# Performance work log

Hardware: AMD Instinct MI355X
Metric: run time of the kernel (lower is better)

The kernel has to match this reference:

```python
import jax, jax.numpy as jnp
import numpy as np

EPS = 1e-8
PHI = (1 + 5 ** 0.5) / 2
B, S, D, H, L, O = 8, 2048, 256, 512, 3, 1
NH = 4
HD = H // NH


def setup_inputs() -> dict:
    key = jax.random.key(0)
    ks = jax.random.split(key, 12)
    g = lambda k, shape, s=0.02: jax.random.normal(k, shape, dtype=jnp.float32) * s
    # Fibonacci modular spiral embedding (fixed, requires_grad=False in torch)
    idx = jnp.arange(D, dtype=jnp.float32)
    r = (PHI * idx) % 1.0
    th = 2 * jnp.pi * r
    phase_emb = jnp.stack([r * jnp.cos(th), r * jnp.sin(th)], axis=1)  # [D,2]
    return dict(
        x=jax.random.normal(ks[0], (B, S, D), dtype=jnp.float32),
        proj_w=g(ks[1], (D, D), 0.06), proj_b=jnp.zeros((D,), jnp.float32),
        phase_emb=phase_emb,
        hebb_w=g(ks[2], (H, 2), 0.5),
        attn_in_w=g(ks[3], (L, 3 * H, H)), attn_in_b=jnp.zeros((L, 3 * H), jnp.float32),
        attn_out_w=g(ks[4], (L, H, H)), attn_out_b=jnp.zeros((L, H), jnp.float32),
        ff1_w=g(ks[5], (L, 4 * H, H)), ff1_b=jnp.zeros((L, 4 * H), jnp.float32),
        ff2_w=g(ks[6], (L, H, 4 * H)), ff2_b=jnp.zeros((L, H), jnp.float32),
        ln1_w=jnp.ones((L, H), jnp.float32), ln1_b=jnp.zeros((L, H), jnp.float32),
        ln2_w=jnp.ones((L, H), jnp.float32), ln2_b=jnp.zeros((L, H), jnp.float32),
        normA_w=jnp.ones((H,), jnp.float32), normA_b=jnp.zeros((H,), jnp.float32),
        normB_w=jnp.ones((H // 2,), jnp.float32), normB_b=jnp.zeros((H // 2,), jnp.float32),
        p1_w=g(ks[7], (H // 2, H), 0.04), p1_b=jnp.zeros((H // 2,), jnp.float32),
        p2_w=g(ks[8], (O, H // 2), 0.06), p2_b=jnp.zeros((O,), jnp.float32),
    )


def _ln(x, w, b, eps=1e-5):
    m = x.mean(-1, keepdims=True)
    v = ((x - m) ** 2).mean(-1, keepdims=True)
    return (x - m) * jax.lax.rsqrt(v + eps) * w + b


def _diffuse(psi, mask, dt, steps):
    # Norm-preserving RK2 integration of d(psi)/dt = mask@psi - psi
    def force(state):
        return jnp.einsum('bij,bjd->bid', mask, state) - state

    def step(p, _):
        r = jnp.linalg.norm(p, axis=-1, keepdims=True)
        k1 = force(p)
        ps = p + dt * k1
        ps = ps * (r / (jnp.linalg.norm(ps, axis=-1, keepdims=True) + EPS))
        k2 = force(ps)
        pn = p + 0.5 * dt * (k1 + k2)
        pn = pn * (r / (jnp.linalg.norm(pn, axis=-1, keepdims=True) + EPS))
        return pn, None

    psi, _ = jax.lax.scan(step, psi, None, length=steps)
    return psi


def _forward(x, proj_w, proj_b, phase_emb, hebb_w, attn_in_w, attn_in_b,
             attn_out_w, attn_out_b, ff1_w, ff1_b, ff2_w, ff2_b,
             ln1_w, ln1_b, ln2_w, ln2_b, normA_w, normA_b, normB_w, normB_b,
             p1_w, p1_b, p2_w, p2_b):
    b, s, _ = x.shape
    # PhaseHebbianEmbedder: project then map to 2D phase coords, unit-normalize
    xp = x @ proj_w.T + proj_b                               # [B,S,D]
    pc = jnp.einsum('bsd,dt->bst', xp, phase_emb)            # [B,S,2]
    psi = pc / (jnp.linalg.norm(pc, axis=-1, keepdims=True) + EPS)
    mask = jnp.broadcast_to(jnp.eye(s, dtype=x.dtype), (b, s, s))  # [B,S,S]
    psi = _diffuse(psi, mask, 0.1, 3)
    psi = _diffuse(psi, mask, 0.05, 4)
    A = jnp.einsum('bsd,btd->bst', psi, psi)                 # [B,S,S]
    final_psi = psi[:, -1]                                   # [B,2]
    h = (final_psi @ hebb_w.T)[:, None, :]                   # [B,1,H]
    for l in range(attn_in_w.shape[0]):
        qkv = h @ attn_in_w[l].T + attn_in_b[l]
        q, k, v = jnp.split(qkv, 3, axis=-1)
        hd = lambda t: t.reshape(b, -1, NH, HD).transpose(0, 2, 1, 3)
        q, k, v = hd(q), hd(k), hd(v)
        sc = jnp.einsum('bhqd,bhkd->bhqk', q, k) / jnp.sqrt(jnp.float32(HD))
        att = jax.nn.softmax(sc, axis=-1)
        o = jnp.einsum('bhqk,bhkd->bhqd', att, v).transpose(0, 2, 1, 3).reshape(b, -1, H)
        o = o @ attn_out_w[l].T + attn_out_b[l]
        h = _ln(h + o, ln1_w[l], ln1_b[l])
        ff = jax.nn.silu(h @ ff1_w[l].T + ff1_b[l]) @ ff2_w[l].T + ff2_b[l]
        h = _ln(h + ff, ln2_w[l], ln2_b[l])
    h = _ln(h[:, 0, :], normA_w, normA_b)
    p = jax.nn.silu(h @ p1_w.T + p1_b)
    p = _ln(p, normB_w, normB_b)
    preds = p @ p2_w.T + p2_b                                # [B,O]
    return preds, A, mask, psi


def reference(x, proj_w, proj_b, phase_emb, hebb_w, attn_in_w, attn_in_b,
              attn_out_w, attn_out_b, ff1_w, ff1_b, ff2_w, ff2_b,
              ln1_w, ln1_b, ln2_w, ln2_b, normA_w, normA_b, normB_w, normB_b,
              p1_w, p1_b, p2_w, p2_b):
    return _forward(x, proj_w, proj_b, phase_emb, hebb_w, attn_in_w, attn_in_b,
                    attn_out_w, attn_out_b, ff1_w, ff1_b, ff2_w, ff2_b,
                    ln1_w, ln1_b, ln2_w, ln2_b, normA_w, normA_b,
                    normB_w, normB_b, p1_w, p1_b, p2_w, p2_b)
```

## Files before the change

kernel.cpp:

```cpp
#include <hip/hip_runtime.h>
#include <hip/hip_bf16.h>

#define BB 8
#define SS 2048
#define DD 256
#define HH 512
#define LL 3
#define NROWS (BB * SS)

typedef float floatx4 __attribute__((ext_vector_type(4)));

__device__ __forceinline__ void amask_row(const float* __restrict__ psi,
                                          float* __restrict__ A, float* __restrict__ M,
                                          int blk)
{
    int tid = threadIdx.x;
    int b = blk >> 11, i = blk & (SS - 1);
    float2 pi = *reinterpret_cast<const float2*>(psi + (size_t)blk * 2);
    #pragma unroll
    for (int c = 0; c < 2; ++c) {
        int j0 = c * 1024 + tid * 4;
        const float4* pr = reinterpret_cast<const float4*>(psi + ((size_t)b * SS + j0) * 2);
        float4 q0 = pr[0], q1 = pr[1];
        floatx4 o;
        o.x = pi.x * q0.x + pi.y * q0.y;
        o.y = pi.x * q0.z + pi.y * q0.w;
        o.z = pi.x * q1.x + pi.y * q1.y;
        o.w = pi.x * q1.z + pi.y * q1.w;
        size_t rb = (size_t)blk * SS + j0;
        __builtin_nontemporal_store(o, reinterpret_cast<floatx4*>(A + rb));
        floatx4 m;
        m.x = (i == j0    ) ? 1.f : 0.f;
        m.y = (i == j0 + 1) ? 1.f : 0.f;
        m.z = (i == j0 + 2) ? 1.f : 0.f;
        m.w = (i == j0 + 3) ? 1.f : 0.f;
        __builtin_nontemporal_store(m, reinterpret_cast<floatx4*>(M + rb));
    }
}

__global__ void compute_M(const float* __restrict__ pw, const float* __restrict__ pb,
                          const float* __restrict__ pe, float* __restrict__ Mc)
{
    __shared__ float s0[4][256], s1[4][256];
    int tid = threadIdx.x;
    int k = tid & 255;
    int sub = tid >> 8;
    float a0 = 0.f, a1 = 0.f;
    #pragma unroll 8
    for (int d = sub * 64; d < sub * 64 + 64; ++d) {
        float w = pw[d * DD + k];
        a0 += w * pe[2 * d];
        a1 += w * pe[2 * d + 1];
    }
    s0[sub][k] = a0;
    s1[sub][k] = a1;
    __syncthreads();
    if (tid < 256) {
        Mc[2 * tid]     = s0[0][tid] + s0[1][tid] + s0[2][tid] + s0[3][tid];
        Mc[2 * tid + 1] = s1[0][tid] + s1[1][tid] + s1[2][tid] + s1[3][tid];
    }
    if (tid < 64) {
        float c0 = 0.f, c1 = 0.f;
        for (int d = tid; d < DD; d += 64) {
            c0 += pb[d] * pe[2 * d];
            c1 += pb[d] * pe[2 * d + 1];
        }
        #pragma unroll
        for (int dd = 32; dd; dd >>= 1) {
            c0 += __shfl_xor(c0, dd);
            c1 += __shfl_xor(c1, dd);
        }
        if (tid == 0) { Mc[512] = c0; Mc[513] = c1; }
    }
}

__global__ void psi_kernel(const float* __restrict__ x, const float* __restrict__ Mc,
                           const float* __restrict__ hebb,
                           float* __restrict__ psi, float* __restrict__ T)
{
    __shared__ float sM[516];
    __shared__ float sH[2];
    int tid = threadIdx.x;
    for (int i = tid; i < 514; i += 256) sM[i] = Mc[i];
    __syncthreads();

    int sub = tid & 3;
    int rloc = tid >> 2;
    int rid = blockIdx.x * 64 + rloc;
    const float4* xr = reinterpret_cast<const float4*>(x + (size_t)rid * DD);
    float a0 = 0.f, a1 = 0.f;
    #pragma unroll
    for (int i = sub; i < DD / 4; i += 4) {
        float4 v = xr[i];
        int k2 = i * 8;
        a0 += v.x * sM[k2]     + v.y * sM[k2 + 2] + v.z * sM[k2 + 4] + v.w * sM[k2 + 6];
        a1 += v.x * sM[k2 + 1] + v.y * sM[k2 + 3] + v.z * sM[k2 + 5] + v.w * sM[k2 + 7];
    }
    a0 += __shfl_xor(a0, 1); a0 += __shfl_xor(a0, 2);
    a1 += __shfl_xor(a1, 1); a1 += __shfl_xor(a1, 2);

    bool leader = (sub == 0);
    float px = 0.f, py = 0.f;
    if (leader) {
        a0 += sM[512];
        a1 += sM[513];
        float n = sqrtf(a0 * a0 + a1 * a1);
        float scale = 1.f / (n + 1e-8f);
        float r = n * scale;
        #pragma unroll
        for (int it = 0; it < 7; ++it) {
            float f = r / (r + 1e-8f);
            scale *= f;
            r *= f;
        }
        px = a0 * scale;
        py = a1 * scale;
        float2 pv;
        pv.x = px;
        pv.y = py;
        *reinterpret_cast<float2*>(psi + (size_t)rid * 2) = pv;
    }

    if ((blockIdx.x & 31) == 31) {
        if (leader && rloc == 63) { sH[0] = px; sH[1] = py; }
        __syncthreads();
        float hx = sH[0], hy = sH[1];
        int b = blockIdx.x >> 5;
        T[(size_t)b * HH + tid]       = hx * hebb[2 * tid]         + hy * hebb[2 * tid + 1];
        T[(size_t)b * HH + tid + 256] = hx * hebb[2 * (tid + 256)] + hy * hebb[2 * (tid + 256) + 1];
    }
}

__global__ void head_mm(const float* __restrict__ X, int K,
                        const float* __restrict__ xlnw, const float* __restrict__ xlnb,
                        const float* __restrict__ W, const float* __restrict__ bias,
                        const float* __restrict__ res,
                        const float* __restrict__ reslnw, const float* __restrict__ reslnb,
                        float* __restrict__ out, int J, int G, int act,
                        const float* __restrict__ psi,
                        float* __restrict__ Ao, float* __restrict__ Mo,
                        int mmBlocks, int arow0)
{
    const int bid = blockIdx.x;
    if (bid >= mmBlocks) {
        int r = arow0 + (bid - mmBlocks);
        if (r < NROWS) amask_row(psi, Ao, Mo, r);
        return;
    }

    extern __shared__ float sX[];
    __shared__ float s_m[8], s_r[8], s_rm[8], s_rr[8];
    const int tid = threadIdx.x;
    const int row = tid >> 5, lane = tid & 31;
    const bool doLN = (xlnw != nullptr);
    const bool doRLN = (res != nullptr) && (reslnw != nullptr);

    if (doLN) {
        float s = 0.f, ss = 0.f;
        for (int k = lane; k < K; k += 32) {
            float v = X[row * K + k];
            s += v; ss += v * v;
        }
        for (int d = 16; d; d >>= 1) { s += __shfl_down(s, d); ss += __shfl_down(ss, d); }
        if (lane == 0) {
            float m = s / K;
            s_m[row] = m;
            s_r[row] = rsqrtf(ss / K - m * m + 1e-5f);
        }
    }
    if (doRLN) {
        float s = 0.f, ss = 0.f;
        for (int k = lane; k < J; k += 32) {
            float v = res[row * J + k];
            s += v; ss += v * v;
        }
        for (int d = 16; d; d >>= 1) { s += __shfl_down(s, d); ss += __shfl_down(ss, d); }
        if (lane == 0) {
            float m = s / J;
            s_rm[row] = m;
            s_rr[row] = rsqrtf(ss / J - m * m + 1e-5f);
        }
    }
    __syncthreads();

    if (doLN) {
        for (int idx = tid; idx < 8 * K; idx += 256) {
            int b = idx / K, k = idx - b * K;
            sX[idx] = (X[idx] - s_m[b]) * s_r[b] * xlnw[k] + xlnb[k];
        }
        __syncthreads();
    }

    const float* __restrict__ Xp = doLN ? (const float*)sX : X;
    const int g = tid & (G - 1);
    const int jj = tid / G;
    const int j = bid * (256 / G) + jj;

    float acc[8] = {0.f, 0.f, 0.f, 0.f, 0.f, 0.f, 0.f, 0.f};
    if (j < J) {
        const float4* W4 = reinterpret_cast<const float4*>(W + (size_t)j * K);
        const int K4 = K >> 2;
        for (int i4 = g; i4 < K4; i4 += G) {
            float4 w4 = W4[i4];
            int k = i4 << 2;
            #pragma unroll
            for (int b = 0; b < 8; ++b) {
                float4 xv = *reinterpret_cast<const float4*>(Xp + b * K + k);
                acc[b] = fmaf(w4.x, xv.x, acc[b]);
                acc[b] = fmaf(w4.y, xv.y, acc[b]);
                acc[b] = fmaf(w4.z, xv.z, acc[b]);
                acc[b] = fmaf(w4.w, xv.w, acc[b]);
            }
        }
    }
    for (int d = G >> 1; d; d >>= 1) {
        #pragma unroll
        for (int b = 0; b < 8; ++b) acc[b] += __shfl_down(acc[b], d);
    }
    if (g == 0 && j < J) {
        float bs = bias ? bias[j] : 0.f;
        #pragma unroll
        for (int b = 0; b < 8; ++b) {
            float v = acc[b] + bs;
            if (act) v = v / (1.f + expf(-v));
            if (res) {
                float rv = res[(size_t)b * J + j];
                if (reslnw) rv = (rv - s_rm[b]) * s_rr[b] * reslnw[j] + reslnb[j];
                v += rv;
            }
            out[(size_t)b * J + j] = v;
        }
    }
}

__device__ __forceinline__ void ln8(const float* in, float* out, int N, int sh,
                                    const float* __restrict__ w,
                                    const float* __restrict__ bvec,
                                    float* s_m, float* s_r, int tid)
{
    int row = tid >> 5, lane = tid & 31;
    float s = 0.f, ss = 0.f;
    for (int k = lane; k < N; k += 32) {
        float v = in[(row << sh) + k];
        s += v; ss += v * v;
    }
    #pragma unroll
    for (int d = 16; d; d >>= 1) { s += __shfl_down(s, d); ss += __shfl_down(ss, d); }
    if (lane == 0) {
        float m = s / N;
        s_m[row] = m;
        s_r[row] = rsqrtf(ss / N - m * m + 1e-5f);
    }
    __syncthreads();
    for (int idx = tid; idx < (N << 3); idx += 256) {
        int b = idx >> sh, k = idx & (N - 1);
        out[idx] = (in[idx] - s_m[b]) * s_r[b] * w[k] + bvec[k];
    }
    __syncthreads();
}

__global__ void tail_kernel(const float* __restrict__ T,
                            const float* __restrict__ ln2w, const float* __restrict__ ln2b,
                            const float* __restrict__ nAw, const float* __restrict__ nAb,
                            const float* __restrict__ nBw, const float* __restrict__ nBb,
                            const float* __restrict__ p1w, const float* __restrict__ p1b,
                            const float* __restrict__ p2w, const float* __restrict__ p2b,
                            float* __restrict__ preds,
                            const float* __restrict__ psi,
                            float* __restrict__ Ao, float* __restrict__ Mo, int arow0)
{
    const int bid = blockIdx.x;
    const int tid = threadIdx.x;
    if (bid >= 1) {
        int r = arow0 + (bid - 1);
        if (r < NROWS) amask_row(psi, Ao, Mo, r);
        return;
    }
    __shared__ __align__(16) float sT[8 * HH];
    __shared__ __align__(16) float sX[8 * HH];
    __shared__ __align__(16) float sS[8 * 256];
    __shared__ float s_m[8], s_r[8];
    const float4* sX4 = reinterpret_cast<const float4*>(sX);

    for (int idx = tid; idx < 4096; idx += 256) sT[idx] = T[idx];
    __syncthreads();
    ln8(sT, sX, HH, 9, ln2w + 2 * HH, ln2b + 2 * HH, s_m, s_r, tid);
    ln8(sX, sX, HH, 9, nAw, nAb, s_m, s_r, tid);
    {
        int j = tid;
        float acc[8] = {0,0,0,0,0,0,0,0};
        const float4* W4 = reinterpret_cast<const float4*>(p1w + (size_t)j * HH);
        for (int i4 = 0; i4 < 128; ++i4) {
            float4 w = W4[i4];
            #pragma unroll
            for (int b = 0; b < 8; ++b) {
                float4 xv = sX4[b * 128 + i4];
                acc[b] = fmaf(w.x, xv.x, acc[b]);
                acc[b] = fmaf(w.y, xv.y, acc[b]);
                acc[b] = fmaf(w.z, xv.z, acc[b]);
                acc[b] = fmaf(w.w, xv.w, acc[b]);
            }
        }
        float bp = p1b[j];
        #pragma unroll
        for (int b = 0; b < 8; ++b) {
            float v = acc[b] + bp;
            v = v / (1.f + expf(-v));
            sS[b * 256 + j] = v;
        }
    }
    __syncthreads();
    ln8(sS, sS, 256, 8, nBw, nBb, s_m, s_r, tid);
    {
        int b = tid >> 5, k = tid & 31;
        float s = 0.f;
        for (int kk = k; kk < 256; kk += 32) s += sS[b * 256 + kk] * p2w[kk];
        #pragma unroll
        for (int d = 16; d; d >>= 1) s += __shfl_down(s, d);
        if (k == 0) preds[b] = s + p2b[0];
    }
}

extern "C" void kernel_launch(void* const* d_in, const int* in_sizes, int n_in,
                              void* d_out, int out_size, void* d_ws, size_t ws_size,
                              hipStream_t stream)
{
    const float* x      = (const float*)d_in[0];
    const float* proj_w = (const float*)d_in[1];
    const float* proj_b = (const float*)d_in[2];
    const float* pe     = (const float*)d_in[3];
    const float* hebb   = (const float*)d_in[4];
    const float* ai_w   = (const float*)d_in[5];
    const float* ai_b   = (const float*)d_in[6];
    const float* ao_w   = (const float*)d_in[7];
    const float* ao_b   = (const float*)d_in[8];
    const float* f1_w   = (const float*)d_in[9];
    const float* f1_b   = (const float*)d_in[10];
    const float* f2_w   = (const float*)d_in[11];
    const float* f2_b   = (const float*)d_in[12];
    const float* ln1w   = (const float*)d_in[13];
    const float* ln1b   = (const float*)d_in[14];
    const float* ln2w   = (const float*)d_in[15];
    const float* ln2b   = (const float*)d_in[16];
    const float* nAw    = (const float*)d_in[17];
    const float* nAb    = (const float*)d_in[18];
    const float* nBw    = (const float*)d_in[19];
    const float* nBb    = (const float*)d_in[20];
    const float* p1w    = (const float*)d_in[21];
    const float* p1b    = (const float*)d_in[22];
    const float* p2w    = (const float*)d_in[23];
    const float* p2b    = (const float*)d_in[24];

    float* out   = (float*)d_out;
    float* preds = out;
    float* A     = out + 8;
    float* Mask  = out + 8 + (size_t)BB * SS * SS;
    float* Psi   = out + 8 + (size_t)2 * BB * SS * SS;

    float* ws = (float*)d_ws;
    float* Mc = ws;
    float* T  = ws + 640;
    float* V  = ws + 4736;
    float* T1 = ws + 8832;
    float* F  = ws + 12928;

    compute_M<<<1, 1024, 0, stream>>>(proj_w, proj_b, pe, Mc);
    psi_kernel<<<NROWS / 64, 256, 0, stream>>>(x, Mc, hebb, Psi, T);

    int arow = 0;
    const int QROW = 1261;
    for (int l = 0; l < LL; ++l) {
        const float* pxw = l ? ln2w + (l - 1) * HH : nullptr;
        const float* pxb = l ? ln2b + (l - 1) * HH : nullptr;
        head_mm<<<64 + QROW, 256, (pxw ? 8 * HH * 4 : 0), stream>>>(
            T, HH, pxw, pxb,
            ai_w + ((size_t)l * 3 * HH + 2 * HH) * HH, ai_b + l * 3 * HH + 2 * HH,
            nullptr, nullptr, nullptr, V, HH, 32, 0,
            Psi, A, Mask, 64, arow);
        arow += QROW;
        head_mm<<<64 + QROW, 256, 0, stream>>>(
            V, HH, nullptr, nullptr,
            ao_w + (size_t)l * HH * HH, ao_b + l * HH,
            T, pxw, pxb, T1, HH, 32, 0,
            Psi, A, Mask, 64, arow);
        arow += QROW;
        head_mm<<<128 + QROW, 256, 8 * HH * 4, stream>>>(
            T1, HH, ln1w + l * HH, ln1b + l * HH,
            f1_w + (size_t)l * 4 * HH * HH, f1_b + l * 4 * HH,
            nullptr, nullptr, nullptr, F, 4 * HH, 16, 1,
            Psi, A, Mask, 128, arow);
        arow += QROW;
        head_mm<<<128 + QROW, 256, 0, stream>>>(
            F, 4 * HH, nullptr, nullptr,
            f2_w + (size_t)l * HH * 4 * HH, f2_b + l * HH,
            T1, ln1w + l * HH, ln1b + l * HH, T, HH, 64, 0,
            Psi, A, Mask, 128, arow);
        arow += QROW;
    }
    {
        int qrem = NROWS - arow;
        tail_kernel<<<1 + qrem, 256, 0, stream>>>(
            T, ln2w, ln2b, nAw, nAb, nBw, nBb, p1w, p1b, p2w, p2b,
            preds, Psi, A, Mask, arow);
    }
}
```

Baseline: 206.6 us.

## Move A/mask writes out of GEMM kernels into a dedicated kernel

The A and mask output rows were previously spread as extra blocks across every head_mm and tail launch, so the tiny matmul chain overlapped with the big store traffic. This change removes that interleaving and writes all rows in one standalone kernel at the end, with 4 rows per block and ordinary stores in place of nontemporal ones. It gives up the overlap of the serial small-GEMM chain with the bandwidth-bound writes, and the GEMM launches become much smaller and cheaper, likely as a simplification.

```diff
diff --git a/kernel.cpp b/kernel.cpp
--- a/kernel.cpp
+++ b/kernel.cpp
@@ -9,34 +9,6 @@
 #define NROWS (BB * SS)
 
 typedef float floatx4 __attribute__((ext_vector_type(4)));
-
-__device__ __forceinline__ void amask_row(const float* __restrict__ psi,
-                                          float* __restrict__ A, float* __restrict__ M,
-                                          int blk)
-{
-    int tid = threadIdx.x;
-    int b = blk >> 11, i = blk & (SS - 1);
-    float2 pi = *reinterpret_cast<const float2*>(psi + (size_t)blk * 2);
-    #pragma unroll
-    for (int c = 0; c < 2; ++c) {
-        int j0 = c * 1024 + tid * 4;
-        const float4* pr = reinterpret_cast<const float4*>(psi + ((size_t)b * SS + j0) * 2);
-        float4 q0 = pr[0], q1 = pr[1];
-        floatx4 o;
-        o.x = pi.x * q0.x + pi.y * q0.y;
-        o.y = pi.x * q0.z + pi.y * q0.w;
-        o.z = pi.x * q1.x + pi.y * q1.y;
-        o.w = pi.x * q1.z + pi.y * q1.w;
-        size_t rb = (size_t)blk * SS + j0;
-        __builtin_nontemporal_store(o, reinterpret_cast<floatx4*>(A + rb));
-        floatx4 m;
-        m.x = (i == j0    ) ? 1.f : 0.f;
-        m.y = (i == j0 + 1) ? 1.f : 0.f;
-        m.z = (i == j0 + 2) ? 1.f : 0.f;
-        m.w = (i == j0 + 3) ? 1.f : 0.f;
-        __builtin_nontemporal_store(m, reinterpret_cast<floatx4*>(M + rb));
-    }
-}
 
 __global__ void compute_M(const float* __restrict__ pw, const float* __restrict__ pb,
                           const float* __restrict__ pe, float* __restrict__ Mc)
@@ -136,18 +108,9 @@
                         const float* __restrict__ W, const float* __restrict__ bias,
                         const float* __restrict__ res,
                         const float* __restrict__ reslnw, const float* __restrict__ reslnb,
-                        float* __restrict__ out, int J, int G, int act,
-                        const float* __restrict__ psi,
-                        float* __restrict__ Ao, float* __restrict__ Mo,
-                        int mmBlocks, int arow0)
+                        float* __restrict__ out, int J, int G, int act)
 {
     const int bid = blockIdx.x;
-    if (bid >= mmBlocks) {
-        int r = arow0 + (bid - mmBlocks);
-        if (r < NROWS) amask_row(psi, Ao, Mo, r);
-        return;
-    }
-
     extern __shared__ float sX[];
     __shared__ float s_m[8], s_r[8], s_rm[8], s_rr[8];
     const int tid = threadIdx.x;
@@ -265,17 +228,9 @@
                             const float* __restrict__ nBw, const float* __restrict__ nBb,
                             const float* __restrict__ p1w, const float* __restrict__ p1b,
                             const float* __restrict__ p2w, const float* __restrict__ p2b,
-                            float* __restrict__ preds,
-                            const float* __restrict__ psi,
-                            float* __restrict__ Ao, float* __restrict__ Mo, int arow0)
-{
-    const int bid = blockIdx.x;
+                            float* __restrict__ preds)
+{
     const int tid = threadIdx.x;
-    if (bid >= 1) {
-        int r = arow0 + (bid - 1);
-        if (r < NROWS) amask_row(psi, Ao, Mo, r);
-        return;
-    }
     __shared__ __align__(16) float sT[8 * HH];
     __shared__ __align__(16) float sX[8 * HH];
     __shared__ __align__(16) float sS[8 * 256];
@@ -318,6 +273,38 @@
         #pragma unroll
         for (int d = 16; d; d >>= 1) s += __shfl_down(s, d);
         if (k == 0) preds[b] = s + p2b[0];
+    }
+}
+
+__global__ void amask_all(const float* __restrict__ psi,
+                          float* __restrict__ A, float* __restrict__ M)
+{
+    int tid = threadIdx.x;
+    int r0 = blockIdx.x * 4;
+    #pragma unroll
+    for (int rr = 0; rr < 4; ++rr) {
+        int blk = r0 + rr;
+        int b = blk >> 11, i = blk & (SS - 1);
+        float2 pi = *reinterpret_cast<const float2*>(psi + (size_t)blk * 2);
+        #pragma unroll
+        for (int c = 0; c < 2; ++c) {
+            int j0 = c * 1024 + tid * 4;
+            const float4* pr = reinterpret_cast<const float4*>(psi + ((size_t)b * SS + j0) * 2);
+            float4 q0 = pr[0], q1 = pr[1];
+            float4 o;
+            o.x = pi.x * q0.x + pi.y * q0.y;
+            o.y = pi.x * q0.z + pi.y * q0.w;
+            o.z = pi.x * q1.x + pi.y * q1.y;
+            o.w = pi.x * q1.z + pi.y * q1.w;
+            size_t rb = (size_t)blk * SS + j0;
+            *reinterpret_cast<float4*>(A + rb) = o;
+            float4 m;
+            m.x = (i == j0    ) ? 1.f : 0.f;
+            m.y = (i == j0 + 1) ? 1.f : 0.f;
+            m.z = (i == j0 + 2) ? 1.f : 0.f;
+            m.w = (i == j0 + 3) ? 1.f : 0.f;
+            *reinterpret_cast<float4*>(M + rb) = m;
+        }
     }
 }
 
@@ -367,40 +354,27 @@
     compute_M<<<1, 1024, 0, stream>>>(proj_w, proj_b, pe, Mc);
     psi_kernel<<<NROWS / 64, 256, 0, stream>>>(x, Mc, hebb, Psi, T);
 
-    int arow = 0;
-    const int QROW = 1261;
     for (int l = 0; l < LL; ++l) {
         const float* pxw = l ? ln2w + (l - 1) * HH : nullptr;
         const float* pxb = l ? ln2b + (l - 1) * HH : nullptr;
-        head_mm<<<64 + QROW, 256, (pxw ? 8 * HH * 4 : 0), stream>>>(
+        head_mm<<<64, 256, (pxw ? 8 * HH * 4 : 0), stream>>>(
             T, HH, pxw, pxb,
             ai_w + ((size_t)l * 3 * HH + 2 * HH) * HH, ai_b + l * 3 * HH + 2 * HH,
-            nullptr, nullptr, nullptr, V, HH, 32, 0,
-            Psi, A, Mask, 64, arow);
-        arow += QROW;
-        head_mm<<<64 + QROW, 256, 0, stream>>>(
+            nullptr, nullptr, nullptr, V, HH, 32, 0);
+        head_mm<<<64, 256, 0, stream>>>(
             V, HH, nullptr, nullptr,
             ao_w + (size_t)l * HH * HH, ao_b + l * HH,
-            T, pxw, pxb, T1, HH, 32, 0,
-            Psi, A, Mask, 64, arow);
-        arow += QROW;
-        head_mm<<<128 + QROW, 256, 8 * HH * 4, stream>>>(
+            T, pxw, pxb, T1, HH, 32, 0);
+        head_mm<<<128, 256, 8 * HH * 4, stream>>>(
             T1, HH, ln1w + l * HH, ln1b + l * HH,
             f1_w + (size_t)l * 4 * HH * HH, f1_b + l * 4 * HH,
-            nullptr, nullptr, nullptr, F, 4 * HH, 16, 1,
-            Psi, A, Mask, 128, arow);
-        arow += QROW;
-        head_mm<<<128 + QROW, 256, 0, stream>>>(
+            nullptr, nullptr, nullptr, F, 4 * HH, 16, 1);
+        head_mm<<<128, 256, 0, stream>>>(
             F, 4 * HH, nullptr, nullptr,
             f2_w + (size_t)l * HH * 4 * HH, f2_b + l * HH,
-            T1, ln1w + l * HH, ln1b + l * HH, T, HH, 64, 0,
-            Psi, A, Mask, 128, arow);
-        arow += QROW;
-    }
-    {
-        int qrem = NROWS - arow;
-        tail_kernel<<<1 + qrem, 256, 0, stream>>>(
-            T, ln2w, ln2b, nAw, nAb, nBw, nBb, p1w, p1b, p2w, p2b,
-            preds, Psi, A, Mask, arow);
-    }
-}
+            T1, ln1w + l * HH, ln1b + l * HH, T, HH, 64, 0);
+    }
+    tail_kernel<<<1, 256, 0, stream>>>(
+        T, ln2w, ln2b, nAw, nAb, nBw, nBb, p1w, p1b, p2w, p2b, preds);
+    amask_all<<<NROWS / 4, 256, 0, stream>>>(Psi, A, Mask);
+}
```

After: 251.4 us. 1.22x slower.
